# Performance work log

Measured on AMD Instinct MI355X. Metric: run time of the kernel, lower is better.

The kernel has to match this reference:

```python
import jax, jax.numpy as jnp
import numpy as np

B, L, D, H = 2, 2048, 1024, 16
HD = D // H  # head_dim = 64


def setup_inputs() -> dict:
    key = jax.random.key(0)
    ks = jax.random.split(key, 9)
    s = 0.02
    return {
        "x": jax.random.normal(ks[0], (B, L, D), dtype=jnp.float32),
        "wq": jax.random.normal(ks[1], (D, D), dtype=jnp.float32) * s,
        "bq": jnp.zeros((D,), dtype=jnp.float32),
        "wk": jax.random.normal(ks[2], (D, D), dtype=jnp.float32) * s,
        "bk": jnp.zeros((D,), dtype=jnp.float32),
        "wv": jax.random.normal(ks[3], (D, D), dtype=jnp.float32) * s,
        "bv": jnp.zeros((D,), dtype=jnp.float32),
        "wo": jax.random.normal(ks[4], (D, D), dtype=jnp.float32) * s,
        "bo": jnp.zeros((D,), dtype=jnp.float32),
    }


def reference(x, wq, bq, wk, bk, wv, bv, wo, bo):
    b, l, d = x.shape
    # projections -> [B, H, L, HD]
    def split_heads(t):
        return t.reshape(b, l, H, HD).transpose(0, 2, 1, 3)
    q = split_heads(x @ wq + bq)
    k = split_heads(x @ wk + bk)
    v = split_heads(x @ wv + bv)
    scores = jnp.einsum('bhqd,bhkd->bhqk', q, k) / jnp.sqrt(jnp.float32(HD))
    # causal mask via -inf then clamp to [-50, 50]: masked entries become -50 (faithful to torch code)
    mask = jnp.triu(jnp.full((l, l), -jnp.inf, dtype=scores.dtype), k=1)
    scores = jnp.clip(scores + mask[None, None, :, :], -50.0, 50.0)
    attn = jax.nn.softmax(scores, axis=-1)
    # dropout is identity in eval/deterministic mode
    out = jnp.einsum('bhqk,bhkd->bhqd', attn, v)
    out = out.transpose(0, 2, 1, 3).reshape(b, l, d)
    out = out @ wo + bo
    return out, attn
```

## Files before the change

kernel.cpp:

```cpp
#include <hip/hip_runtime.h>
#include <hip/hip_bf16.h>

#define B_  2
#define L_  2048
#define D_  1024
#define H_  16
#define HD_ 64

typedef __bf16 bf16x8 __attribute__((ext_vector_type(8)));
typedef float  f32x4  __attribute__((ext_vector_type(4)));
using bf16_t = __hip_bfloat16;
typedef unsigned int u32;
typedef unsigned long long u64;

static __device__ __forceinline__ f32x4 mfma16(bf16x8 a, bf16x8 b, f32x4 c) {
    return __builtin_amdgcn_mfma_f32_16x16x32_bf16(a, b, c, 0, 0, 0);
}

static __device__ __forceinline__ void gl16(const bf16_t* g, bf16_t* l) {
    __builtin_amdgcn_global_load_lds(
        (const __attribute__((address_space(1))) unsigned int*)g,
        (__attribute__((address_space(3))) unsigned int*)l, 16, 0, 0);
}

static __device__ __forceinline__ u32 cvtpk(float lo, float hi) {
    u32 r;
    asm("v_cvt_pk_bf16_f32 %0, %1, %2" : "=v"(r) : "v"(lo), "v"(hi));
    return r;
}

__global__ __launch_bounds__(256) void k_prep(
        const float* __restrict__ x,
        const float* __restrict__ w0, const float* __restrict__ w1,
        const float* __restrict__ w2, const float* __restrict__ w3,
        bf16_t* __restrict__ xb,
        bf16_t* __restrict__ t0, bf16_t* __restrict__ t1,
        bf16_t* __restrict__ t2, bf16_t* __restrict__ t3) {
    __shared__ bf16_t tile[64][65];
    int z = blockIdx.z;
    int t = threadIdx.x;
    if (z >= 4) {
        int slice = z - 4;
        int lin = blockIdx.y * 16 + blockIdx.x;
        int idx = (slice * 256 + lin) * 256 + t;
        const float4* p = (const float4*)x + (size_t)idx * 2;
        float4 a = p[0], b = p[1];
        union { bf16_t h[8]; bf16x8 v; } u;
        u.h[0] = __float2bfloat16(a.x); u.h[1] = __float2bfloat16(a.y);
        u.h[2] = __float2bfloat16(a.z); u.h[3] = __float2bfloat16(a.w);
        u.h[4] = __float2bfloat16(b.x); u.h[5] = __float2bfloat16(b.y);
        u.h[6] = __float2bfloat16(b.z); u.h[7] = __float2bfloat16(b.w);
        *(bf16x8*)(xb + (size_t)idx * 8) = u.v;
        return;
    }
    const float* w = (z == 0) ? w0 : (z == 1) ? w1 : (z == 2) ? w2 : w3;
    bf16_t* wt     = (z == 0) ? t0 : (z == 1) ? t1 : (z == 2) ? t2 : t3;
    int kb = blockIdx.x * 64, nb = blockIdx.y * 64;
    int r  = t >> 4, c4 = (t & 15) * 4;
    #pragma unroll
    for (int it = 0; it < 4; ++it) {
        int kr = r + it * 16;
        float4 v = *(const float4*)&w[(size_t)(kb + kr) * D_ + nb + c4];
        tile[kr][c4 + 0] = __float2bfloat16(v.x);
        tile[kr][c4 + 1] = __float2bfloat16(v.y);
        tile[kr][c4 + 2] = __float2bfloat16(v.z);
        tile[kr][c4 + 3] = __float2bfloat16(v.w);
    }
    __syncthreads();
    #pragma unroll
    for (int it = 0; it < 4; ++it) {
        int nr = r + it * 16;
        union { bf16_t h[4]; u64 u; } o;
        o.h[0] = tile[c4 + 0][nr];
        o.h[1] = tile[c4 + 1][nr];
        o.h[2] = tile[c4 + 2][nr];
        o.h[3] = tile[c4 + 3][nr];
        *(u64*)&wt[(size_t)(nb + nr) * D_ + kb + c4] = o.u;
    }
}

__global__ __launch_bounds__(256, 3) void k_gemm_qkv(
        const bf16_t* __restrict__ A,
        const bf16_t* __restrict__ Wq, const bf16_t* __restrict__ Wk, const bf16_t* __restrict__ Wv,
        const float* __restrict__ bq, const float* __restrict__ bk, const float* __restrict__ bv,
        bf16_t* __restrict__ Qo, bf16_t* __restrict__ Ko, bf16_t* __restrict__ Vo) {
    __shared__ __align__(16) bf16_t Al[128][32];
    __shared__ __align__(16) bf16_t Bl[128][32];
    const int K = D_;
    int z = blockIdx.z;
    const bf16_t* Wt = (z == 0) ? Wq : (z == 1) ? Wk : Wv;
    const float* bias = (z == 0) ? bq : (z == 1) ? bk : bv;
    bf16_t* outp      = (z == 0) ? Qo : (z == 1) ? Ko : Vo;
    int tid = threadIdx.x, lane = tid & 63, wid = tid >> 6;
    int m0 = blockIdx.y * 128, n0 = blockIdx.x * 128;
    int wm = (wid >> 1) * 64, wn = (wid & 1) * 64;
    int r16 = lane & 15, g = lane >> 4;
    int lrow = lane >> 2, lcol = (lane & 3) * 8;
    f32x4 acc[4][4] = {};
    for (int kb = 0; kb < K; kb += 32) {
        __syncthreads();
        gl16(&A [(size_t)(m0 + wid * 32 + lrow) * K + kb + lcol],      &Al[wid * 32][0]);
        gl16(&A [(size_t)(m0 + wid * 32 + 16 + lrow) * K + kb + lcol], &Al[wid * 32 + 16][0]);
        gl16(&Wt[(size_t)(n0 + wid * 32 + lrow) * K + kb + lcol],      &Bl[wid * 32][0]);
        gl16(&Wt[(size_t)(n0 + wid * 32 + 16 + lrow) * K + kb + lcol], &Bl[wid * 32 + 16][0]);
        __syncthreads();
        bf16x8 af[4], bfr[4];
        #pragma unroll
        for (int i = 0; i < 4; ++i) af[i]  = *(const bf16x8*)&Al[wm + i * 16 + r16][g * 8];
        #pragma unroll
        for (int j = 0; j < 4; ++j) bfr[j] = *(const bf16x8*)&Bl[wn + j * 16 + r16][g * 8];
        #pragma unroll
        for (int i = 0; i < 4; ++i)
            #pragma unroll
            for (int j = 0; j < 4; ++j)
                acc[i][j] = mfma16(af[i], bfr[j], acc[i][j]);
    }
    if (z == 2) {
        #pragma unroll
        for (int i = 0; i < 4; ++i)
            #pragma unroll
            for (int j = 0; j < 4; ++j) {
                int n = n0 + wn + j * 16 + r16;
                float bv2 = bias[n];
                int h = n >> 6, hd = n & 63;
                int m = m0 + wm + i * 16 + g * 4;
                int bb = m >> 11, l0 = m & (L_ - 1);
                u32 lo = cvtpk(acc[i][j][0] + bv2, acc[i][j][1] + bv2);
                u32 hi = cvtpk(acc[i][j][2] + bv2, acc[i][j][3] + bv2);
                u64 pk = ((u64)hi << 32) | lo;
                *(u64*)&Vo[(((size_t)(bb * H_ + h)) * HD_ + hd) * L_ + l0] = pk;
            }
    } else {
        #pragma unroll
        for (int i = 0; i < 4; ++i) {
            #pragma unroll
            for (int j = 0; j < 4; ++j) {
                int n = n0 + wn + j * 16 + r16;
                float bv2 = bias[n];
                int h = n >> 6, hd = n & 63;
                #pragma unroll
                for (int e = 0; e < 4; ++e) {
                    int m = m0 + wm + i * 16 + g * 4 + e;
                    float v = acc[i][j][e] + bv2;
                    int bb = m >> 11, l = m & (L_ - 1);
                    outp[(((size_t)(bb * H_ + h)) * L_ + l) * HD_ + hd] = __float2bfloat16(v);
                }
            }
        }
    }
}

__global__ __launch_bounds__(256, 2) void k_gemm_o(const bf16_t* __restrict__ A,
                                                   const bf16_t* __restrict__ Wt,
                                                   const float* __restrict__ bias,
                                                   float* __restrict__ outp) {
    __shared__ __align__(16) bf16_t Al[128][32];
    __shared__ __align__(16) bf16_t Bl[64][32];
    const int K = D_;
    int tid = threadIdx.x, lane = tid & 63, wid = tid >> 6;
    int m0 = blockIdx.y * 128, n0 = blockIdx.x * 64;
    int wm = (wid >> 1) * 64, wn = (wid & 1) * 32;
    int r16 = lane & 15, g = lane >> 4;
    int lrow = lane >> 2, lcol = (lane & 3) * 8;
    f32x4 acc[4][2] = {};
    for (int kb = 0; kb < K; kb += 32) {
        __syncthreads();
        gl16(&A [(size_t)(m0 + wid * 32 + lrow) * K + kb + lcol],      &Al[wid * 32][0]);
        gl16(&A [(size_t)(m0 + wid * 32 + 16 + lrow) * K + kb + lcol], &Al[wid * 32 + 16][0]);
        gl16(&Wt[(size_t)(n0 + wid * 16 + lrow) * K + kb + lcol],      &Bl[wid * 16][0]);
        __syncthreads();
        bf16x8 af[4], bfr[2];
        #pragma unroll
        for (int i = 0; i < 4; ++i) af[i]  = *(const bf16x8*)&Al[wm + i * 16 + r16][g * 8];
        #pragma unroll
        for (int j = 0; j < 2; ++j) bfr[j] = *(const bf16x8*)&Bl[wn + j * 16 + r16][g * 8];
        #pragma unroll
        for (int i = 0; i < 4; ++i)
            #pragma unroll
            for (int j = 0; j < 2; ++j)
                acc[i][j] = mfma16(af[i], bfr[j], acc[i][j]);
    }
    #pragma unroll
    for (int i = 0; i < 4; ++i)
        #pragma unroll
        for (int j = 0; j < 2; ++j) {
            int n = n0 + wn + j * 16 + r16;
            float bv = bias[n];
            #pragma unroll
            for (int e = 0; e < 4; ++e) {
                int m = m0 + wm + i * 16 + g * 4 + e;
                outp[(size_t)m * D_ + n] = acc[i][j][e] + bv;
            }
        }
}

__global__ __launch_bounds__(256, 4) void k_attn(const bf16_t* __restrict__ Q,
                                                 const bf16_t* __restrict__ Kb,
                                                 const bf16_t* __restrict__ VT,
                                                 bf16_t* __restrict__ ctx,
                                                 float* __restrict__ attn) {
    __shared__ __align__(16) bf16_t K_lds[2][64][64];
    __shared__ __align__(16) bf16_t V_lds[2][64][64];
    int tid = threadIdx.x, lane = tid & 63, wid = tid >> 6;
    int bid = blockIdx.x;
    int r   = bid >> 3;
    int jj  = r & 31, s = r >> 5;
    int bh  = (bid & 7) + 8 * s;
    int j2  = (jj + ((s >> 1) << 4)) & 31;
    int qt  = (s & 1) ? (31 - j2) : j2;
    int b = bh >> 4, h = bh & 15;
    int qb = qt * 64;
    const int diag = qt;
    const bf16_t* Qh = Q  + (size_t)bh * L_ * HD_;
    const bf16_t* Kh = Kb + (size_t)bh * L_ * HD_;
    const bf16_t* Vh = VT + (size_t)bh * HD_ * L_;
    int r16 = lane & 15, g = lane >> 4;
    const float scale2 = 0.125f * 1.44269504088896340736f;
    const float clamp2 = 50.0f * 1.44269504088896340736f;
    int qrow0 = qb + wid * 16;
    int qrow  = qrow0 + r16;

    {
        int zs = qb + 64;
        f32x4 z4 = {0.f, 0.f, 0.f, 0.f};
        for (int rr = 0; rr < 16; ++rr) {
            float* rowp = attn + ((size_t)bh * L_ + qrow0 + rr) * L_;
            for (int c = zs + lane * 4; c < L_; c += 256)
                __builtin_nontemporal_store(z4, (f32x4*)&rowp[c]);
        }
    }

    bf16x8 q0 = *(const bf16x8*)&Qh[(size_t)qrow * HD_ + g * 8];
    bf16x8 q1 = *(const bf16x8*)&Qh[(size_t)qrow * HD_ + 32 + g * 8];

    int srow = lane >> 3, sunit = ((lane & 7) ^ (lane >> 3)) * 8;
    auto STAGE_K = [&](int kt1, int nxt) {
        #pragma unroll
        for (int i = 0; i < 2; ++i) {
            int cb = wid * 16 + i * 8;
            gl16(&Kh[(size_t)(kt1 * 64 + cb + srow) * HD_ + sunit], &K_lds[nxt][cb][0]);
        }
    };
    auto STAGE_V = [&](int kt1, int nxt) {
        #pragma unroll
        for (int i = 0; i < 2; ++i) {
            int cb = wid * 16 + i * 8;
            gl16(&Vh[(size_t)(cb + srow) * L_ + kt1 * 64 + sunit], &V_lds[nxt][cb][0]);
        }
    };

    f32x4 ctxa[4] = {};
    float zsum = 0.f;
    int rx = r16 & 7;

    STAGE_K(0, 0); STAGE_V(0, 0);
    int cur = 0;
    for (int kt = 0; kt <= diag; ++kt) {
        __syncthreads();
        int nxt = cur ^ 1;
        if (kt < diag) { STAGE_K(kt + 1, nxt); STAGE_V(kt + 1, nxt); }
        int kb = kt * 64;
        #pragma unroll
        for (int sub = 0; sub < 2; ++sub) {
            f32x4 sa[2];
            #pragma unroll
            for (int sp = 0; sp < 2; ++sp) {
                int krow = sub * 32 + sp * 16 + r16;
                bf16x8 kf0 = *(const bf16x8*)&K_lds[cur][krow][(g ^ rx) * 8];
                bf16x8 kf1 = *(const bf16x8*)&K_lds[cur][krow][((4 + g) ^ rx) * 8];
                f32x4 zz = {};
                sa[sp] = mfma16(kf1, q1, mfma16(kf0, q0, zz));
            }
            int kb2 = kb + sub * 32;
            u32 dw[2][2];
            #pragma unroll
            for (int sp = 0; sp < 2; ++sp) {
                float ev[4];
                #pragma unroll
                for (int e = 0; e < 4; ++e) {
                    int key = kb2 + sp * 16 + g * 4 + e;
                    float sc = fminf(fmaxf(sa[sp][e] * scale2, -clamp2), clamp2);
                    ev[e] = (key > qrow) ? 0.f : exp2f(sc);
                    zsum += ev[e];
                }
                dw[sp][0] = cvtpk(ev[0], ev[1]);
                dw[sp][1] = cvtpk(ev[2], ev[3]);
            }
            union { u32 u[4]; bf16x8 v; } pa;
            pa.u[0] = dw[0][0]; pa.u[1] = dw[0][1];
            pa.u[2] = dw[1][0]; pa.u[3] = dw[1][1];
            #pragma unroll
            for (int t = 0; t < 4; ++t) {
                int vrow = t * 16 + r16;
                int u0 = ((sub * 4 + (g >> 1)) ^ rx) * 8 + (g & 1) * 4;
                int u1 = ((sub * 4 + 2 + (g >> 1)) ^ rx) * 8 + (g & 1) * 4;
                union { u64 d[2]; bf16x8 v; } vf;
                vf.d[0] = *(const u64*)&V_lds[cur][vrow][u0];
                vf.d[1] = *(const u64*)&V_lds[cur][vrow][u1];
                ctxa[t] = mfma16(pa.v, vf.v, ctxa[t]);
            }
        }
        cur = nxt;
    }

    __syncthreads();
    STAGE_K(0, 0);

    float v = zsum;
    v += __shfl_xor(v, 16);
    v += __shfl_xor(v, 32);
    float invz = 1.f / v;

    #pragma unroll
    for (int e = 0; e < 4; ++e) {
        float izq = __shfl(invz, g * 4 + e);
        int qr = qrow0 + g * 4 + e;
        #pragma unroll
        for (int t = 0; t < 4; ++t)
            ctx[((size_t)b * L_ + qr) * D_ + h * HD_ + t * 16 + r16] =
                __float2bfloat16(ctxa[t][e] * izq);
    }

    cur = 0;
    for (int kt = 0; kt <= diag; ++kt) {
        __syncthreads();
        int nxt = cur ^ 1;
        if (kt < diag) STAGE_K(kt + 1, nxt);
        int kb = kt * 64;
        #pragma unroll
        for (int sub = 0; sub < 2; ++sub)
            #pragma unroll
            for (int sp = 0; sp < 2; ++sp) {
                int krow = sub * 32 + sp * 16 + r16;
                bf16x8 kf0 = *(const bf16x8*)&K_lds[cur][krow][(g ^ rx) * 8];
                bf16x8 kf1 = *(const bf16x8*)&K_lds[cur][krow][((4 + g) ^ rx) * 8];
                f32x4 zz = {};
                f32x4 sa = mfma16(kf1, q1, mfma16(kf0, q0, zz));
                int cb = kb + sub * 32 + sp * 16 + g * 4;
                f32x4 fv;
                #pragma unroll
                for (int e = 0; e < 4; ++e) {
                    int key = cb + e;
                    float sc = fminf(fmaxf(sa[e] * scale2, -clamp2), clamp2);
                    fv[e] = (key > qrow) ? 0.f : exp2f(sc) * invz;
                }
                __builtin_nontemporal_store(fv,
                    (f32x4*)&attn[((size_t)bh * L_ + qrow) * L_ + cb]);
            }
        cur = nxt;
    }
}

extern "C" void kernel_launch(void* const* d_in, const int* in_sizes, int n_in,
                              void* d_out, int out_size, void* d_ws, size_t ws_size,
                              hipStream_t stream) {
    const float* x  = (const float*)d_in[0];
    const float* wq = (const float*)d_in[1];
    const float* bq = (const float*)d_in[2];
    const float* wk = (const float*)d_in[3];
    const float* bk = (const float*)d_in[4];
    const float* wv = (const float*)d_in[5];
    const float* bv = (const float*)d_in[6];
    const float* wo = (const float*)d_in[7];
    const float* bo = (const float*)d_in[8];

    char* ws = (char*)d_ws;
    bf16_t* xb   = (bf16_t*)(ws);
    bf16_t* wqt  = (bf16_t*)(ws + ( 8u << 20));
    bf16_t* wkt  = (bf16_t*)(ws + (10u << 20));
    bf16_t* wvt  = (bf16_t*)(ws + (12u << 20));
    bf16_t* wot  = (bf16_t*)(ws + (14u << 20));
    bf16_t* Qb   = (bf16_t*)(ws + (16u << 20));
    bf16_t* Kbuf = (bf16_t*)(ws + (24u << 20));
    bf16_t* VTb  = (bf16_t*)(ws + (32u << 20));
    bf16_t* ctxb = (bf16_t*)(ws + (40u << 20));

    float* out  = (float*)d_out;
    float* attn = out + (size_t)B_ * L_ * D_;

    dim3 gp(16, 16, 12);
    k_prep<<<gp, 256, 0, stream>>>(x, wq, wk, wv, wo, xb, wqt, wkt, wvt, wot);

    dim3 g3(D_ / 128, (B_ * L_) / 128, 3);
    k_gemm_qkv<<<g3, 256, 0, stream>>>(xb, wqt, wkt, wvt, bq, bk, bv, Qb, Kbuf, VTb);

    k_attn<<<1024, 256, 0, stream>>>(Qb, Kbuf, VTb, ctxb, attn);

    dim3 gg(D_ / 64, (B_ * L_) / 128);
    k_gemm_o<<<gg, 256, 0, stream>>>(ctxb, wot, bo, (float*)d_out);
}
```

Measured before the change: 228.7 us.

## Pair complementary causal query tiles in one block to share staged K/V

Each attention block now has 512 threads and covers two query tiles, qt=j and qt=31-j, of the same head. The K/V tiles staged into LDS are shared by both halves, and the causal loop runs to the larger tile's diagonal. The aim is to halve global K/V staging per query tile and balance work evenly across blocks. The trade-off is that the half with the shorter diagonal sits idle at barriers once it finishes, and the bigger block may lower occupancy.

Result: slower. 245.5 us (+7.4%).

```diff
diff --git a/kernel.cpp b/kernel.cpp
--- a/kernel.cpp
+++ b/kernel.cpp
@@ -194,7 +194,7 @@
         }
 }
 
-__global__ __launch_bounds__(256, 4) void k_attn(const bf16_t* __restrict__ Q,
+__global__ __launch_bounds__(512, 4) void k_attn(const bf16_t* __restrict__ Q,
                                                  const bf16_t* __restrict__ Kb,
                                                  const bf16_t* __restrict__ VT,
                                                  bf16_t* __restrict__ ctx,
@@ -204,20 +204,22 @@
     int tid = threadIdx.x, lane = tid & 63, wid = tid >> 6;
     int bid = blockIdx.x;
     int r   = bid >> 3;
-    int jj  = r & 31, s = r >> 5;
+    int s   = r >> 4, j = r & 15;
     int bh  = (bid & 7) + 8 * s;
-    int j2  = (jj + ((s >> 1) << 4)) & 31;
-    int qt  = (s & 1) ? (31 - j2) : j2;
+    int tile = wid >> 2;
+    int wtid = wid & 3;
+    int qt   = tile ? j : (31 - j);
+    int diag = qt;
+    int ktmax = 31 - j;
     int b = bh >> 4, h = bh & 15;
     int qb = qt * 64;
-    const int diag = qt;
     const bf16_t* Qh = Q  + (size_t)bh * L_ * HD_;
     const bf16_t* Kh = Kb + (size_t)bh * L_ * HD_;
     const bf16_t* Vh = VT + (size_t)bh * HD_ * L_;
     int r16 = lane & 15, g = lane >> 4;
     const float scale2 = 0.125f * 1.44269504088896340736f;
     const float clamp2 = 50.0f * 1.44269504088896340736f;
-    int qrow0 = qb + wid * 16;
+    int qrow0 = qb + wtid * 16;
     int qrow  = qrow0 + r16;
 
     {
@@ -235,18 +237,10 @@
 
     int srow = lane >> 3, sunit = ((lane & 7) ^ (lane >> 3)) * 8;
     auto STAGE_K = [&](int kt1, int nxt) {
-        #pragma unroll
-        for (int i = 0; i < 2; ++i) {
-            int cb = wid * 16 + i * 8;
-            gl16(&Kh[(size_t)(kt1 * 64 + cb + srow) * HD_ + sunit], &K_lds[nxt][cb][0]);
-        }
+        gl16(&Kh[(size_t)(kt1 * 64 + 8 * wid + srow) * HD_ + sunit], &K_lds[nxt][8 * wid][0]);
     };
     auto STAGE_V = [&](int kt1, int nxt) {
-        #pragma unroll
-        for (int i = 0; i < 2; ++i) {
-            int cb = wid * 16 + i * 8;
-            gl16(&Vh[(size_t)(cb + srow) * L_ + kt1 * 64 + sunit], &V_lds[nxt][cb][0]);
-        }
+        gl16(&Vh[(size_t)(8 * wid + srow) * L_ + kt1 * 64 + sunit], &V_lds[nxt][8 * wid][0]);
     };
 
     f32x4 ctxa[4] = {};
@@ -255,49 +249,51 @@
 
     STAGE_K(0, 0); STAGE_V(0, 0);
     int cur = 0;
-    for (int kt = 0; kt <= diag; ++kt) {
+    for (int kt = 0; kt <= ktmax; ++kt) {
         __syncthreads();
         int nxt = cur ^ 1;
-        if (kt < diag) { STAGE_K(kt + 1, nxt); STAGE_V(kt + 1, nxt); }
-        int kb = kt * 64;
-        #pragma unroll
-        for (int sub = 0; sub < 2; ++sub) {
-            f32x4 sa[2];
-            #pragma unroll
-            for (int sp = 0; sp < 2; ++sp) {
-                int krow = sub * 32 + sp * 16 + r16;
-                bf16x8 kf0 = *(const bf16x8*)&K_lds[cur][krow][(g ^ rx) * 8];
-                bf16x8 kf1 = *(const bf16x8*)&K_lds[cur][krow][((4 + g) ^ rx) * 8];
-                f32x4 zz = {};
-                sa[sp] = mfma16(kf1, q1, mfma16(kf0, q0, zz));
-            }
-            int kb2 = kb + sub * 32;
-            u32 dw[2][2];
-            #pragma unroll
-            for (int sp = 0; sp < 2; ++sp) {
-                float ev[4];
-                #pragma unroll
-                for (int e = 0; e < 4; ++e) {
-                    int key = kb2 + sp * 16 + g * 4 + e;
-                    float sc = fminf(fmaxf(sa[sp][e] * scale2, -clamp2), clamp2);
-                    ev[e] = (key > qrow) ? 0.f : exp2f(sc);
-                    zsum += ev[e];
-                }
-                dw[sp][0] = cvtpk(ev[0], ev[1]);
-                dw[sp][1] = cvtpk(ev[2], ev[3]);
-            }
-            union { u32 u[4]; bf16x8 v; } pa;
-            pa.u[0] = dw[0][0]; pa.u[1] = dw[0][1];
-            pa.u[2] = dw[1][0]; pa.u[3] = dw[1][1];
-            #pragma unroll
-            for (int t = 0; t < 4; ++t) {
-                int vrow = t * 16 + r16;
-                int u0 = ((sub * 4 + (g >> 1)) ^ rx) * 8 + (g & 1) * 4;
-                int u1 = ((sub * 4 + 2 + (g >> 1)) ^ rx) * 8 + (g & 1) * 4;
-                union { u64 d[2]; bf16x8 v; } vf;
-                vf.d[0] = *(const u64*)&V_lds[cur][vrow][u0];
-                vf.d[1] = *(const u64*)&V_lds[cur][vrow][u1];
-                ctxa[t] = mfma16(pa.v, vf.v, ctxa[t]);
+        if (kt < ktmax) { STAGE_K(kt + 1, nxt); STAGE_V(kt + 1, nxt); }
+        if (kt <= diag) {
+            int kb = kt * 64;
+            #pragma unroll
+            for (int sub = 0; sub < 2; ++sub) {
+                f32x4 sa[2];
+                #pragma unroll
+                for (int sp = 0; sp < 2; ++sp) {
+                    int krow = sub * 32 + sp * 16 + r16;
+                    bf16x8 kf0 = *(const bf16x8*)&K_lds[cur][krow][(g ^ rx) * 8];
+                    bf16x8 kf1 = *(const bf16x8*)&K_lds[cur][krow][((4 + g) ^ rx) * 8];
+                    f32x4 zz = {};
+                    sa[sp] = mfma16(kf1, q1, mfma16(kf0, q0, zz));
+                }
+                int kb2 = kb + sub * 32;
+                u32 dw[2][2];
+                #pragma unroll
+                for (int sp = 0; sp < 2; ++sp) {
+                    float ev[4];
+                    #pragma unroll
+                    for (int e = 0; e < 4; ++e) {
+                        int key = kb2 + sp * 16 + g * 4 + e;
+                        float sc = fminf(fmaxf(sa[sp][e] * scale2, -clamp2), clamp2);
+                        ev[e] = (key > qrow) ? 0.f : exp2f(sc);
+                        zsum += ev[e];
+                    }
+                    dw[sp][0] = cvtpk(ev[0], ev[1]);
+                    dw[sp][1] = cvtpk(ev[2], ev[3]);
+                }
+                union { u32 u[4]; bf16x8 v; } pa;
+                pa.u[0] = dw[0][0]; pa.u[1] = dw[0][1];
+                pa.u[2] = dw[1][0]; pa.u[3] = dw[1][1];
+                #pragma unroll
+                for (int t = 0; t < 4; ++t) {
+                    int vrow = t * 16 + r16;
+                    int u0 = ((sub * 4 + (g >> 1)) ^ rx) * 8 + (g & 1) * 4;
+                    int u1 = ((sub * 4 + 2 + (g >> 1)) ^ rx) * 8 + (g & 1) * 4;
+                    union { u64 d[2]; bf16x8 v; } vf;
+                    vf.d[0] = *(const u64*)&V_lds[cur][vrow][u0];
+                    vf.d[1] = *(const u64*)&V_lds[cur][vrow][u1];
+                    ctxa[t] = mfma16(pa.v, vf.v, ctxa[t]);
+                }
             }
         }
         cur = nxt;
@@ -322,31 +318,33 @@
     }
 
     cur = 0;
-    for (int kt = 0; kt <= diag; ++kt) {
+    for (int kt = 0; kt <= ktmax; ++kt) {
         __syncthreads();
         int nxt = cur ^ 1;
-        if (kt < diag) STAGE_K(kt + 1, nxt);
-        int kb = kt * 64;
-        #pragma unroll
-        for (int sub = 0; sub < 2; ++sub)
-            #pragma unroll
-            for (int sp = 0; sp < 2; ++sp) {
-                int krow = sub * 32 + sp * 16 + r16;
-                bf16x8 kf0 = *(const bf16x8*)&K_lds[cur][krow][(g ^ rx) * 8];
-                bf16x8 kf1 = *(const bf16x8*)&K_lds[cur][krow][((4 + g) ^ rx) * 8];
-                f32x4 zz = {};
-                f32x4 sa = mfma16(kf1, q1, mfma16(kf0, q0, zz));
-                int cb = kb + sub * 32 + sp * 16 + g * 4;
-                f32x4 fv;
-                #pragma unroll
-                for (int e = 0; e < 4; ++e) {
-                    int key = cb + e;
-                    float sc = fminf(fmaxf(sa[e] * scale2, -clamp2), clamp2);
-                    fv[e] = (key > qrow) ? 0.f : exp2f(sc) * invz;
-                }
-                __builtin_nontemporal_store(fv,
-                    (f32x4*)&attn[((size_t)bh * L_ + qrow) * L_ + cb]);
-            }
+        if (kt < ktmax) STAGE_K(kt + 1, nxt);
+        if (kt <= diag) {
+            int kb = kt * 64;
+            #pragma unroll
+            for (int sub = 0; sub < 2; ++sub)
+                #pragma unroll
+                for (int sp = 0; sp < 2; ++sp) {
+                    int krow = sub * 32 + sp * 16 + r16;
+                    bf16x8 kf0 = *(const bf16x8*)&K_lds[cur][krow][(g ^ rx) * 8];
+                    bf16x8 kf1 = *(const bf16x8*)&K_lds[cur][krow][((4 + g) ^ rx) * 8];
+                    f32x4 zz = {};
+                    f32x4 sa = mfma16(kf1, q1, mfma16(kf0, q0, zz));
+                    int cb = kb + sub * 32 + sp * 16 + g * 4;
+                    f32x4 fv;
+                    #pragma unroll
+                    for (int e = 0; e < 4; ++e) {
+                        int key = cb + e;
+                        float sc = fminf(fmaxf(sa[e] * scale2, -clamp2), clamp2);
+                        fv[e] = (key > qrow) ? 0.f : exp2f(sc) * invz;
+                    }
+                    __builtin_nontemporal_store(fv,
+                        (f32x4*)&attn[((size_t)bh * L_ + qrow) * L_ + cb]);
+                }
+        }
         cur = nxt;
     }
 }
@@ -384,7 +382,7 @@
     dim3 g3(D_ / 128, (B_ * L_) / 128, 3);
     k_gemm_qkv<<<g3, 256, 0, stream>>>(xb, wqt, wkt, wvt, bq, bk, bv, Qb, Kbuf, VTb);
 
-    k_attn<<<1024, 256, 0, stream>>>(Qb, Kbuf, VTb, ctxb, attn);
+    k_attn<<<512, 512, 0, stream>>>(Qb, Kbuf, VTb, ctxb, attn);
 
     dim3 gg(D_ / 64, (B_ * L_) / 128);
     k_gemm_o<<<gg, 256, 0, stream>>>(ctxb, wot, bo, (float*)d_out);
```
